# Performance work log

Hardware: AMD Instinct MI355X
Metric: run time of the kernel (lower is better)

## Reference

```python
import jax, jax.numpy as jnp
import numpy as np

N_NODES = 100000
N_EDGES = 800000


def setup_inputs() -> dict:
    key = jax.random.key(0)
    ks = jax.random.split(key, 8)
    s = 0.05  # weight scale
    return {
        "x": jax.random.normal(ks[0], (N_NODES, 64), dtype=jnp.float32),
        "edge_index": jax.random.randint(ks[1], (2, N_EDGES), 0, N_NODES, dtype=jnp.int64),
        "eps1": jnp.zeros((), jnp.float32),
        "eps2": jnp.zeros((), jnp.float32),
        "W1a": jax.random.normal(ks[2], (64, 128), dtype=jnp.float32) * s,
        "b1a": jnp.zeros((128,), jnp.float32),
        "W1b": jax.random.normal(ks[3], (128, 128), dtype=jnp.float32) * s,
        "b1b": jnp.zeros((128,), jnp.float32),
        "W2a": jax.random.normal(ks[4], (128, 128), dtype=jnp.float32) * s,
        "b2a": jnp.zeros((128,), jnp.float32),
        "W2b": jax.random.normal(ks[5], (128, 64), dtype=jnp.float32) * s,
        "b2b": jnp.zeros((64,), jnp.float32),
    }


def _gin_conv(h, src, dst, eps, Wa, ba, Wb, bb, n_nodes):
    # sum-aggregate neighbor messages h[src] at dst, add (1+eps)*self
    agg = jax.ops.segment_sum(h[src], dst, num_segments=n_nodes)  # [N, d]
    z = (1.0 + eps) * h + agg
    # MLP: Linear -> ReLU -> Linear (weights stored [in, out])
    return jnp.maximum(z @ Wa + ba, 0.0) @ Wb + bb


def reference(x, edge_index, eps1, eps2, W1a, b1a, W1b, b1b, W2a, b2a, W2b, b2b):
    src, dst = edge_index[0], edge_index[1]
    n = x.shape[0]
    h = _gin_conv(x, src, dst, eps1, W1a, b1a, W1b, b1b, n)
    h = jnp.maximum(h, 0.0)  # outer ReLU; dropout is identity in eval
    out = _gin_conv(h, src, dst, eps2, W2a, b2a, W2b, b2b, n)
    return out
```

## Files before the change

### kernel.cpp

```cpp
#include <hip/hip_runtime.h>
#include <cstdint>

constexpr int CAPA = 15;
constexpr int CAPB = 16;
constexpr int CAP = CAPA + CAPB;
constexpr int FIX = 15;

typedef __attribute__((ext_vector_type(8))) __bf16 bf16x8;
typedef __attribute__((ext_vector_type(16))) float f32x16;
typedef _Float16 f16x2 __attribute__((ext_vector_type(2)));

__device__ __forceinline__ unsigned short f2bf(float f) {
    unsigned int u = __builtin_bit_cast(unsigned int, f);
    u += 0x7fffu + ((u >> 16) & 1u);
    return (unsigned short)(u >> 16);
}
__device__ __forceinline__ float bf2f(unsigned short h) {
    unsigned int u = ((unsigned int)h) << 16;
    return __builtin_bit_cast(float, u);
}
__device__ __forceinline__ unsigned short f2h(float f) {
    _Float16 h = (_Float16)f;
    return __builtin_bit_cast(unsigned short, h);
}
__device__ __forceinline__ float h2f(unsigned short u) {
    return (float)__builtin_bit_cast(_Float16, u);
}
__device__ __forceinline__ float2 h2f2(unsigned int u) {
    f16x2 h = __builtin_bit_cast(f16x2, u);
    return make_float2((float)h.x, (float)h.y);
}


__global__ void zero_kernel(int* __restrict__ bktA, int n) {
    int i = blockIdx.x * 256 + threadIdx.x;
    if (i < n) bktA[(unsigned int)i * 16u] = 0;
}


__global__ void build_kernel(const int* __restrict__ eidx, int E,
                             int* __restrict__ bktA, int* __restrict__ bktB,
                             const float* __restrict__ W1a, const float* __restrict__ W1b,
                             const float* __restrict__ W2a, const float* __restrict__ W2b,
                             unsigned short* __restrict__ wpk,
                             const float* __restrict__ x, unsigned short* __restrict__ xf16,
                             int N) {
    const int gi = blockIdx.x * 256 + threadIdx.x;
    const int stride = gridDim.x * 256;

    for (int e = gi; e < E; e += stride) {
        int s = eidx[e];
        int d = eidx[E + e];
        int pos = atomicAdd(&bktA[(unsigned int)d * 16u], 1);
        if (pos < CAPA) {
            bktA[(unsigned int)d * 16u + 1u + pos] = s;
        } else if (pos < CAP) {
            bktB[(unsigned int)d * 16u + (pos - CAPA)] = s;
        }
    }

    if (gi < 49152) {
        const float* W;
        int K, Nn, base, rel;
        if (gi < 8192) {
            W = W1a; K = 64; Nn = 128; base = 0; rel = gi;
        } else if (gi < 24576) {
            W = W1b; K = 128; Nn = 128; base = 16384; rel = gi - 8192;
        } else if (gi < 40960) {
            W = W2a; K = 128; Nn = 128; base = 49152; rel = gi - 24576;
        } else {
            W = W2b; K = 128; Nn = 64; base = 81920; rel = gi - 40960;
        }
        int j = rel & 7;
        int lane = (rel >> 3) & 63;
        int rest = rel >> 9;
        int ksteps = K / 16;
        int kstep = rest % ksteps;
        int ntile = rest / ksteps;
        int k = kstep * 16 + ((lane >> 5) << 3) + j;
        int ncol = ntile * 32 + (lane & 31);
        float v = W[k * Nn + ncol];
        unsigned short h = f2bf(v);
        unsigned short l = f2bf(v - bf2f(h));
        wpk[base + rel] = h;
        wpk[base + K * Nn + rel] = l;
    }

    const int total4 = N * 16;
    for (int t = gi; t < total4; t += stride) {
        float4 v = ((const float4*)x)[t];
        ushort4 o;
        o.x = f2h(v.x);
        o.y = f2h(v.y);
        o.z = f2h(v.z);
        o.w = f2h(v.w);
        ((ushort4*)xf16)[t] = o;
    }
}


template <int KIN, int KMID, int KOUT, bool RELU_OUT, bool SELF_F32, bool F16_OUT>
__global__ __launch_bounds__(256, 8) void gin_layer_kernel(
    const unsigned short* __restrict__ gf16, const float* __restrict__ hf32,
    const int* __restrict__ bktA, const int* __restrict__ bktB,
    const float* __restrict__ eps,
    const unsigned short* __restrict__ Wahi, const unsigned short* __restrict__ Walo,
    const float* __restrict__ ba,
    const unsigned short* __restrict__ Wbhi, const unsigned short* __restrict__ Wblo,
    const float* __restrict__ bb, float* __restrict__ out_f32,
    unsigned short* __restrict__ outf16, int n) {
    constexpr int ZS = KIN + 8;
    constexpr int TS = KMID + 8;
    constexpr int KSB = KIN / 16;
    constexpr int KSC = KMID / 16;
    __shared__ __align__(16) unsigned short smem[2 * 32 * (KMID + 8)];
    unsigned short* const zhi = smem;
    unsigned short* const zlo = smem + 32 * ZS;
    unsigned short* const thi = smem;
    unsigned short* const tlo = smem + 32 * TS;

    const int tid = threadIdx.x;
    const int lane = tid & 63;
    const int base = blockIdx.x * 32;
    const float scale = 1.0f + eps[0];
    const int wq = __builtin_amdgcn_readfirstlane(tid >> 6);

    float h0x, h0y;
    if (KIN == 64) {
        h0x = h2f(gf16[lane]);
        h0y = 0.f;
    } else {
        float2 t0 = h2f2(((const unsigned int*)gf16)[lane]);
        h0x = t0.x;
        h0y = t0.y;
    }

#pragma unroll
    for (int mi = 0; mi < 8; ++mi) {
        const int m = wq * 8 + mi;
        const int node = base + m;
        const int nc = node < n ? node : n - 1;
        const int* __restrict__ rowA = bktA + (unsigned int)nc * 16u;
        const int cl0 = __builtin_amdgcn_readfirstlane(rowA[0]);
        const int cl = cl0 < CAP ? cl0 : CAP;

        int sIdx[FIX];
#pragma unroll
        for (int j = 0; j < FIX; ++j) {
            int sj = rowA[1 + j];
            sIdx[j] = j < cl ? sj : 0;
        }

        if (KIN == 64) {
            _Float16 p0 = (_Float16)0, p1 = (_Float16)0, p2 = (_Float16)0;
#pragma unroll
            for (int j = 0; j < 5; ++j) {
                p0 += __builtin_bit_cast(_Float16, gf16[(unsigned int)sIdx[j] * 64u + lane]);
                p1 += __builtin_bit_cast(_Float16, gf16[(unsigned int)sIdx[5 + j] * 64u + lane]);
                p2 += __builtin_bit_cast(_Float16, gf16[(unsigned int)sIdx[10 + j] * 64u + lane]);
            }
            float self;
            if (SELF_F32) {
                self = hf32[(unsigned int)nc * 64u + lane];
            } else {
                self = h2f(gf16[(unsigned int)nc * 64u + lane]);
            }
            float res = scale * self;
            res += ((float)p0 + (float)p1) + (float)p2;
            float corr = (float)(FIX - (cl < FIX ? cl : FIX));
            res = __builtin_fmaf(-corr, h0x, res);
            for (int e = FIX; e < cl; ++e)
                res += h2f(gf16[(unsigned int)bktB[(unsigned int)nc * 16u + (e - FIX)] * 64u +
                               lane]);
            unsigned short rh = f2bf(res);
            zhi[m * ZS + lane] = rh;
            zlo[m * ZS + lane] = f2bf(res - bf2f(rh));
        } else {
            const unsigned int* g32 = (const unsigned int*)gf16;
            f16x2 q0 = {(_Float16)0, (_Float16)0};
            f16x2 q1 = q0, q2 = q0;
#pragma unroll
            for (int j = 0; j < 5; ++j) {
                q0 += __builtin_bit_cast(f16x2, g32[(unsigned int)sIdx[j] * 64u + lane]);
                q1 += __builtin_bit_cast(f16x2, g32[(unsigned int)sIdx[5 + j] * 64u + lane]);
                q2 += __builtin_bit_cast(f16x2, g32[(unsigned int)sIdx[10 + j] * 64u + lane]);
            }
            float sx, sy;
            if (SELF_F32) {
                const float2* h2 = (const float2*)hf32;
                float2 a = h2[(unsigned int)nc * 64u + lane];
                sx = a.x;
                sy = a.y;
            } else {
                float2 a = h2f2(g32[(unsigned int)nc * 64u + lane]);
                sx = a.x;
                sy = a.y;
            }
            float ax = scale * sx + (((float)q0.x + (float)q1.x) + (float)q2.x);
            float ay = scale * sy + (((float)q0.y + (float)q1.y) + (float)q2.y);
            float corr = (float)(FIX - (cl < FIX ? cl : FIX));
            ax = __builtin_fmaf(-corr, h0x, ax);
            ay = __builtin_fmaf(-corr, h0y, ay);
            for (int e = FIX; e < cl; ++e) {
                float2 v =
                    h2f2(g32[(unsigned int)bktB[(unsigned int)nc * 16u + (e - FIX)] * 64u + lane]);
                ax += v.x;
                ay += v.y;
            }
            unsigned short hx = f2bf(ax), hy = f2bf(ay);
            unsigned short lx = f2bf(ax - bf2f(hx)), ly = f2bf(ay - bf2f(hy));
            *(unsigned int*)(zhi + m * ZS + 2 * lane) = (unsigned int)hx | ((unsigned int)hy << 16);
            *(unsigned int*)(zlo + m * ZS + 2 * lane) = (unsigned int)lx | ((unsigned int)ly << 16);
        }
    }
    __syncthreads();

    const int r31 = lane & 31;
    const int q = lane >> 5;

    {
        const int nt = wq;
        f32x16 acc;
#pragma unroll
        for (int i = 0; i < 16; ++i) acc[i] = 0.0f;
        const unsigned short* Ah = zhi + r31 * ZS + q * 8;
        const unsigned short* Al = zlo + r31 * ZS + q * 8;
        const unsigned short* Bh = Wahi + ((size_t)(nt * KSB) * 64 + lane) * 8;
        const unsigned short* Bl = Walo + ((size_t)(nt * KSB) * 64 + lane) * 8;
#pragma unroll
        for (int ks = 0; ks < KSB; ++ks) {
            bf16x8 ah = *reinterpret_cast<const bf16x8*>(Ah + ks * 16);
            bf16x8 al = *reinterpret_cast<const bf16x8*>(Al + ks * 16);
            bf16x8 bh = *reinterpret_cast<const bf16x8*>(Bh + ks * 512);
            bf16x8 bl = *reinterpret_cast<const bf16x8*>(Bl + ks * 512);
            acc = __builtin_amdgcn_mfma_f32_32x32x16_bf16(ah, bh, acc, 0, 0, 0);
            acc = __builtin_amdgcn_mfma_f32_32x32x16_bf16(ah, bl, acc, 0, 0, 0);
            acc = __builtin_amdgcn_mfma_f32_32x32x16_bf16(al, bh, acc, 0, 0, 0);
        }
        const int col = nt * 32 + r31;
        const float bias = ba[col];
        unsigned short th_r[16], tl_r[16];
#pragma unroll
        for (int i = 0; i < 16; ++i) {
            float v = fmaxf(acc[i] + bias, 0.0f);
            unsigned short hh = f2bf(v);
            th_r[i] = hh;
            tl_r[i] = f2bf(v - bf2f(hh));
        }
        __syncthreads();
#pragma unroll
        for (int i = 0; i < 16; ++i) {
            const int m = (i & 3) + 8 * (i >> 2) + 4 * q;
            thi[m * TS + col] = th_r[i];
            tlo[m * TS + col] = tl_r[i];
        }
    }
    __syncthreads();

    {
        constexpr int NKS = (KOUT == 64) ? (KSC / 2) : KSC;
        const int nt = (KOUT == 64) ? (wq & 1) : wq;
        const int k0 = (KOUT == 64) ? ((wq >> 1) * NKS) : 0;
        f32x16 acc;
#pragma unroll
        for (int i = 0; i < 16; ++i) acc[i] = 0.0f;
        const unsigned short* Ah = thi + r31 * TS + q * 8 + k0 * 16;
        const unsigned short* Al = tlo + r31 * TS + q * 8 + k0 * 16;
        const unsigned short* Bh = Wbhi + ((size_t)(nt * KSC + k0) * 64 + lane) * 8;
        const unsigned short* Bl = Wblo + ((size_t)(nt * KSC + k0) * 64 + lane) * 8;
#pragma unroll
        for (int ks = 0; ks < NKS; ++ks) {
            bf16x8 ah = *reinterpret_cast<const bf16x8*>(Ah + ks * 16);
            bf16x8 al = *reinterpret_cast<const bf16x8*>(Al + ks * 16);
            bf16x8 bh = *reinterpret_cast<const bf16x8*>(Bh + ks * 512);
            bf16x8 bl = *reinterpret_cast<const bf16x8*>(Bl + ks * 512);
            acc = __builtin_amdgcn_mfma_f32_32x32x16_bf16(ah, bh, acc, 0, 0, 0);
            acc = __builtin_amdgcn_mfma_f32_32x32x16_bf16(ah, bl, acc, 0, 0, 0);
            acc = __builtin_amdgcn_mfma_f32_32x32x16_bf16(al, bh, acc, 0, 0, 0);
        }
        const int col = nt * 32 + r31;
        if (KOUT == 64) {
            __syncthreads();
            float* stg = (float*)smem;
            if (wq >= 2) {
                float* d = stg + ((wq - 2) * 64 + lane) * 20;
#pragma unroll
                for (int c = 0; c < 4; ++c) {
                    float4 v = make_float4(acc[4 * c + 0], acc[4 * c + 1], acc[4 * c + 2],
                                           acc[4 * c + 3]);
                    *reinterpret_cast<float4*>(d + c * 4) = v;
                }
            }
            __syncthreads();
            if (wq < 2) {
                const float* s = stg + (wq * 64 + lane) * 20;
#pragma unroll
                for (int i = 0; i < 16; ++i) acc[i] += s[i];
                const float bias = bb[col];
#pragma unroll
                for (int i = 0; i < 16; ++i) {
                    const int m = (i & 3) + 8 * (i >> 2) + 4 * q;
                    const int node = base + m;
                    if (node < n) {
                        float v = acc[i] + bias;
                        if (RELU_OUT) v = fmaxf(v, 0.0f);
                        out_f32[(size_t)node * KOUT + col] = v;
                    }
                }
            }
        } else {
            const float bias = bb[col];
#pragma unroll
            for (int i = 0; i < 16; ++i) {
                const int m = (i & 3) + 8 * (i >> 2) + 4 * q;
                const int node = base + m;
                if (node < n) {
                    float v = acc[i] + bias;
                    if (RELU_OUT) v = fmaxf(v, 0.0f);
                    if (F16_OUT) {
                        outf16[(size_t)node * KOUT + col] = f2h(v);
                    } else {
                        out_f32[(size_t)node * KOUT + col] = v;
                    }
                }
            }
        }
    }
}


extern "C" void kernel_launch(void* const* d_in, const int* in_sizes, int n_in,
                              void* d_out, int out_size, void* d_ws, size_t ws_size,
                              hipStream_t stream) {
    const float* x = (const float*)d_in[0];
    const int* eidx = (const int*)d_in[1];
    const float* eps1 = (const float*)d_in[2];
    const float* eps2 = (const float*)d_in[3];
    const float* W1a = (const float*)d_in[4];
    const float* b1a = (const float*)d_in[5];
    const float* W1b = (const float*)d_in[6];
    const float* b1b = (const float*)d_in[7];
    const float* W2a = (const float*)d_in[8];
    const float* b2a = (const float*)d_in[9];
    const float* W2b = (const float*)d_in[10];
    const float* b2b = (const float*)d_in[11];
    float* out = (float*)d_out;

    int N = in_sizes[0] / 64;
    int E = in_sizes[1] / 2;

    char* p = (char*)d_ws;
    auto alloc = [&](size_t bytes) {
        char* r = p;
        p += (bytes + 255) & ~(size_t)255;
        return r;
    };
    int* bktA = (int*)alloc((size_t)N * 16 * 4);
    int* bktB = (int*)alloc((size_t)N * 16 * 4);
    unsigned short* h1f = (unsigned short*)alloc((size_t)N * 128 * 2);
    unsigned short* xf16 = (unsigned short*)alloc((size_t)N * 64 * 2);
    unsigned short* wpk = (unsigned short*)alloc(98304 * 2);

    int zb = (N + 255) / 256;
    int eb = (E + 255) / 256;
    int gb = (N + 31) / 32;

    zero_kernel<<<zb, 256, 0, stream>>>(bktA, N);
    build_kernel<<<eb, 256, 0, stream>>>(eidx, E, bktA, bktB, W1a, W1b, W2a, W2b, wpk, x, xf16, N);

    gin_layer_kernel<64, 128, 128, true, true, true><<<gb, 256, 0, stream>>>(
        xf16, x, bktA, bktB, eps1, wpk + 0, wpk + 8192, b1a, wpk + 16384, wpk + 32768, b1b,
        (float*)nullptr, h1f, N);
    gin_layer_kernel<128, 128, 64, false, false, false><<<gb, 256, 0, stream>>>(
        h1f, (const float*)nullptr, bktA, bktB, eps2, wpk + 49152, wpk + 65536, b2a, wpk + 81920,
        wpk + 90112, b2b, out, (unsigned short*)nullptr, N);
}
```

Measured before the change: 220.5 us.

## Fuse setup and both GIN layers into one cooperative persistent kernel

Replaces the zero, build and two layer launches with a single cooperative kernel that uses grid-wide syncs between phases. Layer tiles are processed in a grid-stride loop over 2048 resident blocks. The aim is to remove inter-kernel launch gaps and drain/fill tails. The cost is grid barrier overhead and uneven tile counts per block, and the old multi-kernel path is kept as a fallback if the cooperative launch fails.

```diff
diff --git a/kernel.cpp b/kernel.cpp
--- a/kernel.cpp
+++ b/kernel.cpp
@@ -1,5 +1,8 @@
 #include <hip/hip_runtime.h>
+#include <hip/hip_cooperative_groups.h>
 #include <cstdint>
+
+namespace cg = cooperative_groups;
 
 constexpr int CAPA = 15;
 constexpr int CAPB = 16;
@@ -32,23 +35,9 @@
 }
 
 
-__global__ void zero_kernel(int* __restrict__ bktA, int n) {
-    int i = blockIdx.x * 256 + threadIdx.x;
-    if (i < n) bktA[(unsigned int)i * 16u] = 0;
-}
-
-
-__global__ void build_kernel(const int* __restrict__ eidx, int E,
-                             int* __restrict__ bktA, int* __restrict__ bktB,
-                             const float* __restrict__ W1a, const float* __restrict__ W1b,
-                             const float* __restrict__ W2a, const float* __restrict__ W2b,
-                             unsigned short* __restrict__ wpk,
-                             const float* __restrict__ x, unsigned short* __restrict__ xf16,
-                             int N) {
-    const int gi = blockIdx.x * 256 + threadIdx.x;
-    const int stride = gridDim.x * 256;
-
-    for (int e = gi; e < E; e += stride) {
+__device__ __forceinline__ void bin_edges(int gi, int gstride, const int* __restrict__ eidx,
+                                          int E, int* __restrict__ bktA, int* __restrict__ bktB) {
+    for (int e = gi; e < E; e += gstride) {
         int s = eidx[e];
         int d = eidx[E + e];
         int pos = atomicAdd(&bktA[(unsigned int)d * 16u], 1);
@@ -58,7 +47,13 @@
             bktB[(unsigned int)d * 16u + (pos - CAPA)] = s;
         }
     }
-
+}
+
+__device__ __forceinline__ void pack_weights(int gi, const float* __restrict__ W1a,
+                                             const float* __restrict__ W1b,
+                                             const float* __restrict__ W2a,
+                                             const float* __restrict__ W2b,
+                                             unsigned short* __restrict__ wpk) {
     if (gi < 49152) {
         const float* W;
         int K, Nn, base, rel;
@@ -85,9 +80,12 @@
         wpk[base + rel] = h;
         wpk[base + K * Nn + rel] = l;
     }
-
+}
+
+__device__ __forceinline__ void convert_x(int gi, int gstride, int N, const float* __restrict__ x,
+                                          unsigned short* __restrict__ xf16) {
     const int total4 = N * 16;
-    for (int t = gi; t < total4; t += stride) {
+    for (int t = gi; t < total4; t += gstride) {
         float4 v = ((const float4*)x)[t];
         ushort4 o;
         o.x = f2h(v.x);
@@ -100,28 +98,26 @@
 
 
 template <int KIN, int KMID, int KOUT, bool RELU_OUT, bool SELF_F32, bool F16_OUT>
-__global__ __launch_bounds__(256, 8) void gin_layer_kernel(
-    const unsigned short* __restrict__ gf16, const float* __restrict__ hf32,
-    const int* __restrict__ bktA, const int* __restrict__ bktB,
-    const float* __restrict__ eps,
-    const unsigned short* __restrict__ Wahi, const unsigned short* __restrict__ Walo,
-    const float* __restrict__ ba,
-    const unsigned short* __restrict__ Wbhi, const unsigned short* __restrict__ Wblo,
-    const float* __restrict__ bb, float* __restrict__ out_f32,
-    unsigned short* __restrict__ outf16, int n) {
+__device__ void gin_tile(unsigned short* __restrict__ smem, int base,
+                         const unsigned short* __restrict__ gf16, const float* __restrict__ hf32,
+                         const int* __restrict__ bktA, const int* __restrict__ bktB,
+                         const float* __restrict__ eps,
+                         const unsigned short* __restrict__ Wahi,
+                         const unsigned short* __restrict__ Walo, const float* __restrict__ ba,
+                         const unsigned short* __restrict__ Wbhi,
+                         const unsigned short* __restrict__ Wblo, const float* __restrict__ bb,
+                         float* __restrict__ out_f32, unsigned short* __restrict__ outf16, int n,
+                         int tid) {
     constexpr int ZS = KIN + 8;
     constexpr int TS = KMID + 8;
     constexpr int KSB = KIN / 16;
     constexpr int KSC = KMID / 16;
-    __shared__ __align__(16) unsigned short smem[2 * 32 * (KMID + 8)];
     unsigned short* const zhi = smem;
     unsigned short* const zlo = smem + 32 * ZS;
     unsigned short* const thi = smem;
     unsigned short* const tlo = smem + 32 * TS;
 
-    const int tid = threadIdx.x;
     const int lane = tid & 63;
-    const int base = blockIdx.x * 32;
     const float scale = 1.0f + eps[0];
     const int wq = __builtin_amdgcn_readfirstlane(tid >> 6);
 
@@ -326,6 +322,87 @@
             }
         }
     }
+}
+
+
+struct FusedArgs {
+    const int* eidx;
+    int E;
+    int* bktA;
+    int* bktB;
+    const float *W1a, *W1b, *W2a, *W2b;
+    unsigned short* wpk;
+    const float* x;
+    unsigned short* xf16;
+    unsigned short* h1f;
+    const float *eps1, *eps2, *b1a, *b1b, *b2a, *b2b;
+    float* out;
+    int N;
+};
+
+__global__ __launch_bounds__(256, 8) void fused_kernel(FusedArgs a) {
+    cg::grid_group grid = cg::this_grid();
+    const int tid = threadIdx.x;
+    const int gi = blockIdx.x * 256 + tid;
+    const int gstride = gridDim.x * 256;
+    __shared__ __align__(16) unsigned short smem[2 * 32 * 136];
+
+    for (int i = gi; i < a.N; i += gstride) a.bktA[(unsigned int)i * 16u] = 0;
+    grid.sync();
+
+    bin_edges(gi, gstride, a.eidx, a.E, a.bktA, a.bktB);
+    pack_weights(gi, a.W1a, a.W1b, a.W2a, a.W2b, a.wpk);
+    convert_x(gi, gstride, a.N, a.x, a.xf16);
+    grid.sync();
+
+    const int ntiles = (a.N + 31) / 32;
+    for (int t = blockIdx.x; t < ntiles; t += gridDim.x) {
+        gin_tile<64, 128, 128, true, true, true>(
+            smem, t * 32, a.xf16, a.x, a.bktA, a.bktB, a.eps1, a.wpk + 0, a.wpk + 8192, a.b1a,
+            a.wpk + 16384, a.wpk + 32768, a.b1b, nullptr, a.h1f, a.N, tid);
+        __syncthreads();
+    }
+    grid.sync();
+
+    for (int t = blockIdx.x; t < ntiles; t += gridDim.x) {
+        gin_tile<128, 128, 64, false, false, false>(
+            smem, t * 32, a.h1f, nullptr, a.bktA, a.bktB, a.eps2, a.wpk + 49152, a.wpk + 65536,
+            a.b2a, a.wpk + 81920, a.wpk + 90112, a.b2b, a.out, nullptr, a.N, tid);
+        __syncthreads();
+    }
+}
+
+
+__global__ void zero_kernel(int* __restrict__ bktA, int n) {
+    int i = blockIdx.x * 256 + threadIdx.x;
+    if (i < n) bktA[(unsigned int)i * 16u] = 0;
+}
+
+__global__ void build_kernel(const int* __restrict__ eidx, int E, int* __restrict__ bktA,
+                             int* __restrict__ bktB, const float* __restrict__ W1a,
+                             const float* __restrict__ W1b, const float* __restrict__ W2a,
+                             const float* __restrict__ W2b, unsigned short* __restrict__ wpk,
+                             const float* __restrict__ x, unsigned short* __restrict__ xf16,
+                             int N) {
+    const int gi = blockIdx.x * 256 + threadIdx.x;
+    const int gstride = gridDim.x * 256;
+    bin_edges(gi, gstride, eidx, E, bktA, bktB);
+    pack_weights(gi, W1a, W1b, W2a, W2b, wpk);
+    convert_x(gi, gstride, N, x, xf16);
+}
+
+template <int KIN, int KMID, int KOUT, bool RELU_OUT, bool SELF_F32, bool F16_OUT>
+__global__ __launch_bounds__(256, 8) void gin_layer_kernel(
+    const unsigned short* __restrict__ gf16, const float* __restrict__ hf32,
+    const int* __restrict__ bktA, const int* __restrict__ bktB, const float* __restrict__ eps,
+    const unsigned short* __restrict__ Wahi, const unsigned short* __restrict__ Walo,
+    const float* __restrict__ ba, const unsigned short* __restrict__ Wbhi,
+    const unsigned short* __restrict__ Wblo, const float* __restrict__ bb,
+    float* __restrict__ out_f32, unsigned short* __restrict__ outf16, int n) {
+    __shared__ __align__(16) unsigned short smem[2 * 32 * 136];
+    gin_tile<KIN, KMID, KOUT, RELU_OUT, SELF_F32, F16_OUT>(
+        smem, blockIdx.x * 32, gf16, hf32, bktA, bktB, eps, Wahi, Walo, ba, Wbhi, Wblo, bb,
+        out_f32, outf16, n, threadIdx.x);
 }
 
 
@@ -361,13 +438,31 @@
     unsigned short* xf16 = (unsigned short*)alloc((size_t)N * 64 * 2);
     unsigned short* wpk = (unsigned short*)alloc(98304 * 2);
 
+    static int g_coop = -1;
+    if (g_coop != 0) {
+        FusedArgs a;
+        a.eidx = eidx; a.E = E; a.bktA = bktA; a.bktB = bktB;
+        a.W1a = W1a; a.W1b = W1b; a.W2a = W2a; a.W2b = W2b;
+        a.wpk = wpk; a.x = x; a.xf16 = xf16; a.h1f = h1f;
+        a.eps1 = eps1; a.eps2 = eps2; a.b1a = b1a; a.b1b = b1b; a.b2a = b2a; a.b2b = b2b;
+        a.out = out; a.N = N;
+        void* kargs[] = {&a};
+        hipError_t rc = hipLaunchCooperativeKernel((void*)fused_kernel, dim3(2048), dim3(256),
+                                                   kargs, 0, stream);
+        if (rc == hipSuccess) {
+            g_coop = 1;
+            return;
+        }
+        g_coop = 0;
+        (void)hipGetLastError();
+    }
+
     int zb = (N + 255) / 256;
     int eb = (E + 255) / 256;
     int gb = (N + 31) / 32;
 
     zero_kernel<<<zb, 256, 0, stream>>>(bktA, N);
     build_kernel<<<eb, 256, 0, stream>>>(eidx, E, bktA, bktB, W1a, W1b, W2a, W2b, wpk, x, xf16, N);
-
     gin_layer_kernel<64, 128, 128, true, true, true><<<gb, 256, 0, stream>>>(
         xf16, x, bktA, bktB, eps1, wpk + 0, wpk + 8192, b1a, wpk + 16384, wpk + 32768, b1b,
         (float*)nullptr, h1f, N);
```

Result: slower. 327.4 us (+48.5%).
